# Optimization experiments

Measured on AMD Instinct MI355X. Metric: run time of the kernel, lower is better.

Reference implementation:

```python
import jax, jax.numpy as jnp
import numpy as np

N_NODES = 50000
N_EDGES = 800000
IN_DIM = 128
HEADS = 4
CH = 16            # hidden_dim per head
HC = HEADS * CH    # 64
N_GRAPHS = 64
NEG_SLOPE = 0.2


def gat_layer(x, edge_index, edge_attr, W, We, att_src, att_dst, att_edge, bias):
    """PyG GATConv (concat=True, edge_dim=1, eval mode: no dropout)."""
    N = x.shape[0]
    src, dst = edge_index[0], edge_index[1]
    xs = (x @ W).reshape(N, HEADS, CH)                         # [N,H,C]
    a_src = jnp.sum(xs * att_src, axis=-1)                     # [N,H]
    a_dst = jnp.sum(xs * att_dst, axis=-1)                     # [N,H]
    e = (edge_attr @ We).reshape(-1, HEADS, CH)                # [E,H,C]
    a_edge = jnp.sum(e * att_edge, axis=-1)                    # [E,H]
    alpha = a_src[src] + a_dst[dst] + a_edge                   # [E,H]
    alpha = jax.nn.leaky_relu(alpha, NEG_SLOPE)
    # segment softmax over incoming edges of each dst node
    seg_max = jax.ops.segment_max(alpha, dst, num_segments=N)  # [N,H]
    ealpha = jnp.exp(alpha - seg_max[dst])
    seg_sum = jax.ops.segment_sum(ealpha, dst, num_segments=N)
    coef = ealpha / seg_sum[dst]                               # [E,H]
    msg = xs[src] * coef[:, :, None]                           # [E,H,C]
    out = jax.ops.segment_sum(msg, dst, num_segments=N)        # [N,H,C]
    return out.reshape(N, HC) + bias


def setup_inputs() -> dict:
    key = jax.random.key(0)
    ks = jax.random.split(key, 20)
    s = 0.1
    inp = {
        "x": jax.random.normal(ks[0], (N_NODES, IN_DIM), dtype=jnp.float32),
        "edge_index": jax.random.randint(ks[1], (2, N_EDGES), 0, N_NODES, dtype=jnp.int32),
        "edge_attr": jax.random.normal(ks[2], (N_EDGES, 1), dtype=jnp.float32),
        "batch": jnp.sort(jax.random.randint(ks[3], (N_NODES,), 0, N_GRAPHS, dtype=jnp.int32)),
        # layer 1 params
        "W1": jax.random.normal(ks[4], (IN_DIM, HC), dtype=jnp.float32) * s,
        "We1": jax.random.normal(ks[5], (1, HC), dtype=jnp.float32) * s,
        "as1": jax.random.normal(ks[6], (HEADS, CH), dtype=jnp.float32) * s,
        "ad1": jax.random.normal(ks[7], (HEADS, CH), dtype=jnp.float32) * s,
        "ae1": jax.random.normal(ks[8], (HEADS, CH), dtype=jnp.float32) * s,
        "b1": jnp.zeros((HC,), dtype=jnp.float32),
        # layer 2 params (input HC)
        "W2": jax.random.normal(ks[9], (HC, HC), dtype=jnp.float32) * s,
        "We2": jax.random.normal(ks[10], (1, HC), dtype=jnp.float32) * s,
        "as2": jax.random.normal(ks[11], (HEADS, CH), dtype=jnp.float32) * s,
        "ad2": jax.random.normal(ks[12], (HEADS, CH), dtype=jnp.float32) * s,
        "ae2": jax.random.normal(ks[13], (HEADS, CH), dtype=jnp.float32) * s,
        "b2": jnp.zeros((HC,), dtype=jnp.float32),
    }
    return inp


def reference(x, edge_index, edge_attr, batch,
              W1, We1, as1, ad1, ae1, b1,
              W2, We2, as2, ad2, ae2, b2):
    h = gat_layer(x, edge_index, edge_attr, W1, We1, as1, ad1, ae1, b1)
    h = jax.nn.relu(h)                                          # dropout = identity (eval)
    h = gat_layer(h, edge_index, edge_attr, W2, We2, as2, ad2, ae2, b2)
    # global mean pool per graph
    sums = jax.ops.segment_sum(h, batch, num_segments=N_GRAPHS)           # [G,HC]
    cnt = jax.ops.segment_sum(jnp.ones((h.shape[0],), h.dtype), batch,
                              num_segments=N_GRAPHS)
    return sums / jnp.maximum(cnt, 1.0)[:, None]
```

## Files before the change

### kernel.cpp

```cpp
#include <hip/hip_runtime.h>
#include <hip/hip_fp16.h>
#include <float.h>

#define N_NODES   50000
#define N_EDGES   800000
#define INDIM1    128
#define HC        64
#define N_GRAPHS  64
#define NEG_SLOPE 0.2f
#define CAP       64
#define CSTRIDE   16

#define FGROUPS   521
#define FTBLK     (3 * FGROUPS)
#define FSBLK     (2 * FGROUPS)
#define FGRID     (5 * FGROUPS + 1)
#define ESTRIDE   (FSBLK * 256)

typedef _Float16 feat_t;

__global__ __launch_bounds__(256, 4) void fused1_kernel(const float* __restrict__ x,
                                                        const float* __restrict__ W,
                                                        const float* __restrict__ att_s,
                                                        const float* __restrict__ att_d,
                                                        feat_t* __restrict__ xs,
                                                        float* __restrict__ a_src,
                                                        float* __restrict__ a_dst,
                                                        const int* __restrict__ src,
                                                        const int* __restrict__ dst,
                                                        const float* __restrict__ eattr,
                                                        int* __restrict__ cursor,
                                                        unsigned int* __restrict__ csr_se,
                                                        const float* __restrict__ We1,
                                                        const float* __restrict__ ae1,
                                                        const float* __restrict__ We2,
                                                        const float* __restrict__ ae2,
                                                        float* __restrict__ wd) {
    constexpr int K4 = INDIM1 / 4;
    constexpr int NPW = 8;
    __shared__ float4 Wsh[K4 * 64];
    __shared__ float4 xsh[4][2][K4];
    int bid = blockIdx.x;
    int t = threadIdx.x;

    if (bid == FGRID - 1) {
        if (t < 128) {
            const float* We = (t < 64) ? We1 : We2;
            const float* ae = (t < 64) ? ae1 : ae2;
            int l = t & 63;
            float p = We[l] * ae[l];
            for (int off = 1; off < 16; off <<= 1) p += __shfl_xor(p, off);
            if ((l & 15) == 0) wd[(t >> 6) * 4 + (l >> 4)] = p;
        }
        return;
    }

    int grp = bid / 5;
    int rem = bid - grp * 5;
    if (rem >= 3) {
        int sb = grp * 2 + (rem - 3);
        for (int e = sb * 256 + t; e < N_EDGES; e += ESTRIDE) {
            int d = dst[e];
            int c = atomicAdd(&cursor[(size_t)d * CSTRIDE], 1);
            if (c < CAP) {
                unsigned int pk = (unsigned int)(src[e] & 0xFFFF)
                                | ((unsigned int)__half_as_ushort(__float2half(eattr[e])) << 16);
                csr_se[(size_t)d * CAP + c] = pk;
            }
        }
        return;
    }

    int tb = grp * 3 + rem;
    for (int i = t; i < K4 * 64; i += 256) {
        int k4 = i >> 6, col = i & 63;
        Wsh[i] = make_float4(W[(4 * k4 + 0) * 64 + col], W[(4 * k4 + 1) * 64 + col],
                             W[(4 * k4 + 2) * 64 + col], W[(4 * k4 + 3) * 64 + col]);
    }
    __syncthreads();
    int w = t >> 6, lane = t & 63;
    float avs = att_s[lane], avd = att_d[lane];
    int node0 = tb * (4 * NPW) + w * NPW;
    for (int ng = 0; ng < NPW; ng += 2) {
        int nbase = node0 + ng;
        if (nbase >= N_NODES) return;
        for (int q = lane; q < 2 * K4; q += 64) {
            int nn = q / K4, kk = q - nn * K4;
            int node = nbase + nn;
            xsh[w][nn][kk] = (node < N_NODES)
                ? ((const float4*)(x + (size_t)node * INDIM1))[kk]
                : make_float4(0.f, 0.f, 0.f, 0.f);
        }
        float acc0 = 0.f, acc1 = 0.f;
#pragma unroll 4
        for (int k4 = 0; k4 < K4; ++k4) {
            float4 wv = Wsh[k4 * 64 + lane];
            float4 x0 = xsh[w][0][k4];
            float4 x1 = xsh[w][1][k4];
            acc0 = fmaf(x0.x, wv.x, acc0);
            acc0 = fmaf(x0.y, wv.y, acc0);
            acc0 = fmaf(x0.z, wv.z, acc0);
            acc0 = fmaf(x0.w, wv.w, acc0);
            acc1 = fmaf(x1.x, wv.x, acc1);
            acc1 = fmaf(x1.y, wv.y, acc1);
            acc1 = fmaf(x1.z, wv.z, acc1);
            acc1 = fmaf(x1.w, wv.w, acc1);
        }
#pragma unroll
        for (int nn = 0; nn < 2; ++nn) {
            int node = nbase + nn;
            if (node >= N_NODES) break;
            float a = nn ? acc1 : acc0;
            xs[(size_t)node * 64 + lane] = (feat_t)a;
            float ps = a * avs;
            float pd = a * avd;
            for (int off = 1; off < 16; off <<= 1) {
                ps += __shfl_xor(ps, off);
                pd += __shfl_xor(pd, off);
            }
            if ((lane & 15) == 0) {
                a_src[node * 4 + (lane >> 4)] = ps;
                a_dst[node * 4 + (lane >> 4)] = pd;
            }
        }
    }
}

__global__ __launch_bounds__(256, 4) void agg1_kernel(const feat_t* __restrict__ xs,
                                                      const unsigned int* __restrict__ csr_se,
                                                      const int* __restrict__ degp,
                                                      const float* __restrict__ a_src,
                                                      const float* __restrict__ a_dst,
                                                      const float* __restrict__ wd,
                                                      const float* __restrict__ bias,
                                                      const float* __restrict__ W2,
                                                      const float* __restrict__ as2,
                                                      const float* __restrict__ ad2,
                                                      feat_t* __restrict__ xs2,
                                                      float* __restrict__ asrc2,
                                                      float* __restrict__ adst2) {
    __shared__ float W2sh[64 * 64];
    __shared__ float hshA[4][64];
    __shared__ float hshB[4][64];
    int t = threadIdx.x;
#pragma unroll
    for (int i = 0; i < 4; ++i)
        ((float4*)W2sh)[t + 256 * i] = ((const float4*)W2)[t + 256 * i];

    int w = t >> 6, lane = t & 63;
    const int e_idx = lane >> 2;
    const int h4 = lane & 3;
    const int h2 = lane >> 4;
    int nodeA = blockIdx.x * 8 + w * 2;
    int nodeB = nodeA + 1;

    float wdv = wd[h4];
    float bv = bias[lane];
    float avs2 = as2[lane], avd2 = ad2[lane];
    float advA = a_dst[nodeA * 4 + h4];
    float advB = a_dst[nodeB * 4 + h4];
    int nA = min(degp[(size_t)nodeA * CSTRIDE], CAP);
    int nB = min(degp[(size_t)nodeB * CSTRIDE], CAP);
    int begA = nodeA * CAP, endA = begA + nA;
    int begB = nodeB * CAP, endB = begB + nB;

    float mA = -FLT_MAX, sA = 0.f, accA = 0.f;
    float mB = -FLT_MAX, sB = 0.f, accB = 0.f;

    auto alpha_phase = [&](int beg, int end, int it, float adv,
                           float& m, float& s, float& acc, int& sv, float& wgt) {
        int j = beg + it * 16 + e_idx;
        bool v = j < end;
        sv = 0;
        float a = -FLT_MAX;
        if (v) {
            unsigned int se = csr_se[j];
            sv = (int)(se & 0xFFFFu);
            float ea = __half2float(__ushort_as_half((unsigned short)(se >> 16)));
            float as = a_src[sv * 4 + h4];
            a = as + adv + ea * wdv;
            a = a > 0.f ? a : NEG_SLOPE * a;
        }
        float cm = a;
        cm = fmaxf(cm, __shfl_xor(cm, 4));
        cm = fmaxf(cm, __shfl_xor(cm, 8));
        cm = fmaxf(cm, __shfl_xor(cm, 16));
        cm = fmaxf(cm, __shfl_xor(cm, 32));
        float mn = fmaxf(m, cm);
        float sc = __expf(m - mn);
        wgt = __expf(a - mn);
        s = s * sc + wgt;
        m = mn;
        acc *= __shfl(sc, h2);
    };
    auto gather_phase = [&](int sv, float wgt, float& acc) {
#pragma unroll
        for (int e = 0; e < 16; ++e) {
            int svb = __builtin_amdgcn_readlane(sv, e << 2);
            float wg = __shfl(wgt, (e << 2) | h2);
            acc = fmaf(wg, (float)xs[(size_t)svb * 64 + lane], acc);
        }
    };

    int itA = (nA + 15) >> 4, itB = (nB + 15) >> 4;
    int itC = min(itA, itB);
    for (int it = 0; it < itC; ++it) {
        int svA, svB; float wgtA, wgtB;
        alpha_phase(begA, endA, it, advA, mA, sA, accA, svA, wgtA);
        alpha_phase(begB, endB, it, advB, mB, sB, accB, svB, wgtB);
        gather_phase(svA, wgtA, accA);
        gather_phase(svB, wgtB, accB);
    }
    for (int it = itC; it < itA; ++it) {
        int svA; float wgtA;
        alpha_phase(begA, endA, it, advA, mA, sA, accA, svA, wgtA);
        gather_phase(svA, wgtA, accA);
    }
    for (int it = itC; it < itB; ++it) {
        int svB; float wgtB;
        alpha_phase(begB, endB, it, advB, mB, sB, accB, svB, wgtB);
        gather_phase(svB, wgtB, accB);
    }

    auto finish = [&](float s, float acc) {
        s += __shfl_xor(s, 4);
        s += __shfl_xor(s, 8);
        s += __shfl_xor(s, 16);
        s += __shfl_xor(s, 32);
        float sh = __shfl(s, h2);
        float res = (sh > 0.f) ? acc / sh : 0.f;
        return res + bv;
    };
    float hA = fmaxf(finish(sA, accA), 0.f);
    float hB = fmaxf(finish(sB, accB), 0.f);

    hshA[w][lane] = hA;
    hshB[w][lane] = hB;
    __syncthreads();

    float acc2A = 0.f, acc2B = 0.f;
#pragma unroll
    for (int k4 = 0; k4 < 16; ++k4) {
        float4 ha = ((const float4*)hshA[w])[k4];
        float4 hb = ((const float4*)hshB[w])[k4];
        float w0 = W2sh[(4 * k4 + 0) * 64 + lane];
        float w1 = W2sh[(4 * k4 + 1) * 64 + lane];
        float w2 = W2sh[(4 * k4 + 2) * 64 + lane];
        float w3 = W2sh[(4 * k4 + 3) * 64 + lane];
        acc2A = fmaf(ha.x, w0, acc2A); acc2B = fmaf(hb.x, w0, acc2B);
        acc2A = fmaf(ha.y, w1, acc2A); acc2B = fmaf(hb.y, w1, acc2B);
        acc2A = fmaf(ha.z, w2, acc2A); acc2B = fmaf(hb.z, w2, acc2B);
        acc2A = fmaf(ha.w, w3, acc2A); acc2B = fmaf(hb.w, w3, acc2B);
    }
    xs2[(size_t)nodeA * 64 + lane] = (feat_t)acc2A;
    xs2[(size_t)nodeB * 64 + lane] = (feat_t)acc2B;
    float psA = acc2A * avs2, pdA = acc2A * avd2;
    float psB = acc2B * avs2, pdB = acc2B * avd2;
    for (int off = 1; off < 16; off <<= 1) {
        psA += __shfl_xor(psA, off);
        pdA += __shfl_xor(pdA, off);
        psB += __shfl_xor(psB, off);
        pdB += __shfl_xor(pdB, off);
    }
    if ((lane & 15) == 0) {
        asrc2[nodeA * 4 + (lane >> 4)] = psA;
        adst2[nodeA * 4 + (lane >> 4)] = pdA;
        asrc2[nodeB * 4 + (lane >> 4)] = psB;
        adst2[nodeB * 4 + (lane >> 4)] = pdB;
    }
}

__global__ __launch_bounds__(256, 6) void agg2_kernel(const feat_t* __restrict__ xs,
                                                      const unsigned int* __restrict__ csr_se,
                                                      const int* __restrict__ degp,
                                                      const float* __restrict__ a_src,
                                                      const float* __restrict__ a_dst,
                                                      const float* __restrict__ wd,
                                                      const float* __restrict__ bias,
                                                      const int* __restrict__ batch,
                                                      float* __restrict__ gout) {
    __shared__ float plds[256];
    int t = threadIdx.x;
    int w = t >> 6, lane = t & 63;
    const int e_idx = lane >> 2;
    const int h4 = lane & 3;
    const int h2 = lane >> 4;
    int nodeA = blockIdx.x * 8 + w * 2;
    int nodeB = nodeA + 1;

    float wdv = wd[h4];
    float bv = bias[lane];
    float advA = a_dst[nodeA * 4 + h4];
    float advB = a_dst[nodeB * 4 + h4];
    int nA = min(degp[(size_t)nodeA * CSTRIDE], CAP);
    int nB = min(degp[(size_t)nodeB * CSTRIDE], CAP);
    int begA = nodeA * CAP, endA = begA + nA;
    int begB = nodeB * CAP, endB = begB + nB;

    float mA = -FLT_MAX, sA = 0.f, accA = 0.f;
    float mB = -FLT_MAX, sB = 0.f, accB = 0.f;

    auto alpha_phase = [&](int beg, int end, int it, float adv,
                           float& m, float& s, float& acc, int& sv, float& wgt) {
        int j = beg + it * 16 + e_idx;
        bool v = j < end;
        sv = 0;
        float a = -FLT_MAX;
        if (v) {
            unsigned int se = csr_se[j];
            sv = (int)(se & 0xFFFFu);
            float ea = __half2float(__ushort_as_half((unsigned short)(se >> 16)));
            float as = a_src[sv * 4 + h4];
            a = as + adv + ea * wdv;
            a = a > 0.f ? a : NEG_SLOPE * a;
        }
        float cm = a;
        cm = fmaxf(cm, __shfl_xor(cm, 4));
        cm = fmaxf(cm, __shfl_xor(cm, 8));
        cm = fmaxf(cm, __shfl_xor(cm, 16));
        cm = fmaxf(cm, __shfl_xor(cm, 32));
        float mn = fmaxf(m, cm);
        float sc = __expf(m - mn);
        wgt = __expf(a - mn);
        s = s * sc + wgt;
        m = mn;
        acc *= __shfl(sc, h2);
    };
    auto gather_phase = [&](int sv, float wgt, float& acc) {
#pragma unroll
        for (int e = 0; e < 16; ++e) {
            int svb = __builtin_amdgcn_readlane(sv, e << 2);
            float wg = __shfl(wgt, (e << 2) | h2);
            acc = fmaf(wg, (float)xs[(size_t)svb * 64 + lane], acc);
        }
    };

    int itA = (nA + 15) >> 4, itB = (nB + 15) >> 4;
    int itC = min(itA, itB);
    for (int it = 0; it < itC; ++it) {
        int svA, svB; float wgtA, wgtB;
        alpha_phase(begA, endA, it, advA, mA, sA, accA, svA, wgtA);
        alpha_phase(begB, endB, it, advB, mB, sB, accB, svB, wgtB);
        gather_phase(svA, wgtA, accA);
        gather_phase(svB, wgtB, accB);
    }
    for (int it = itC; it < itA; ++it) {
        int svA; float wgtA;
        alpha_phase(begA, endA, it, advA, mA, sA, accA, svA, wgtA);
        gather_phase(svA, wgtA, accA);
    }
    for (int it = itC; it < itB; ++it) {
        int svB; float wgtB;
        alpha_phase(begB, endB, it, advB, mB, sB, accB, svB, wgtB);
        gather_phase(svB, wgtB, accB);
    }

    auto finish = [&](float s, float acc) {
        s += __shfl_xor(s, 4);
        s += __shfl_xor(s, 8);
        s += __shfl_xor(s, 16);
        s += __shfl_xor(s, 32);
        float sh = __shfl(s, h2);
        float res = (sh > 0.f) ? acc / sh : 0.f;
        return res + bv;
    };
    float resA = finish(sA, accA);
    float resB = finish(sB, accB);

    int gA = batch[nodeA], gB = batch[nodeB];
    int gF = batch[blockIdx.x * 8];
    int gL = batch[blockIdx.x * 8 + 7];
    if (gF == gL) {
        plds[w * 64 + lane] = resA + resB;
        __syncthreads();
        if (w == 0) {
            float v = plds[lane] + plds[64 + lane] +
                      plds[128 + lane] + plds[192 + lane];
            atomicAdd(&gout[gF * 64 + lane], v);
        }
    } else {
        if (gA == gB) {
            atomicAdd(&gout[gA * 64 + lane], resA + resB);
        } else {
            atomicAdd(&gout[gA * 64 + lane], resA);
            atomicAdd(&gout[gB * 64 + lane], resB);
        }
    }
}

__global__ void pool_div_kernel(float* __restrict__ out, const int* __restrict__ batch) {
    int g = blockIdx.x, t = threadIdx.x;
    int lo = 0, hi = N_NODES;
    while (lo < hi) { int mid = (lo + hi) >> 1; if (batch[mid] < g) lo = mid + 1; else hi = mid; }
    int lo2 = lo, hi2 = N_NODES;
    while (lo2 < hi2) { int mid = (lo2 + hi2) >> 1; if (batch[mid] <= g) lo2 = mid + 1; else hi2 = mid; }
    float c = (float)max(lo2 - lo, 1);
    out[g * 64 + t] /= c;
}


extern "C" void kernel_launch(void* const* d_in, const int* in_sizes, int n_in,
                              void* d_out, int out_size, void* d_ws, size_t ws_size,
                              hipStream_t stream) {
    const float* x    = (const float*)d_in[0];
    const int*   eidx = (const int*)d_in[1];
    const float* eat  = (const float*)d_in[2];
    const int*   batch= (const int*)d_in[3];
    const float* W1   = (const float*)d_in[4];
    const float* We1  = (const float*)d_in[5];
    const float* as1  = (const float*)d_in[6];
    const float* ad1  = (const float*)d_in[7];
    const float* ae1  = (const float*)d_in[8];
    const float* b1   = (const float*)d_in[9];
    const float* W2   = (const float*)d_in[10];
    const float* We2  = (const float*)d_in[11];
    const float* as2  = (const float*)d_in[12];
    const float* ad2  = (const float*)d_in[13];
    const float* ae2  = (const float*)d_in[14];
    const float* b2   = (const float*)d_in[15];
    const int* src  = eidx;
    const int* dstp = eidx + N_EDGES;
    float* out = (float*)d_out;

    char* p = (char*)d_ws;
    auto alloc = [&](size_t bytes) {
        char* r = p;
        p += (bytes + 255) & ~(size_t)255;
        return r;
    };
    unsigned int* csrse = (unsigned int*)alloc((size_t)N_NODES * CAP * 4);
    feat_t* xs     = (feat_t*)alloc((size_t)N_NODES * 64 * 2);
    feat_t* hbuf   = (feat_t*)alloc((size_t)N_NODES * 64 * 2);
    float*  asrc   = (float*)alloc((size_t)N_NODES * 4 * 4);
    float*  adst   = (float*)alloc((size_t)N_NODES * 4 * 4);
    float*  asrc2  = (float*)alloc((size_t)N_NODES * 4 * 4);
    float*  adst2  = (float*)alloc((size_t)N_NODES * 4 * 4);
    float*  wd     = (float*)alloc(64);
    int*    cursor = (int*)alloc((size_t)N_NODES * CSTRIDE * 4);

    hipMemsetAsync(cursor, 0, (size_t)N_NODES * CSTRIDE * 4, stream);
    hipMemsetAsync(d_out, 0, (size_t)N_GRAPHS * 64 * 4, stream);

    const int NB = N_NODES / 8;

    fused1_kernel<<<FGRID, 256, 0, stream>>>(x, W1, as1, ad1, xs, asrc, adst,
                                             src, dstp, eat, cursor, csrse,
                                             We1, ae1, We2, ae2, wd);
    agg1_kernel<<<NB, 256, 0, stream>>>(xs, csrse, cursor, asrc, adst,
                                        wd, b1, W2, as2, ad2,
                                        hbuf, asrc2, adst2);
    agg2_kernel<<<NB, 256, 0, stream>>>(hbuf, csrse, cursor, asrc2, adst2,
                                        wd + 4, b2, batch, out);
    pool_div_kernel<<<N_GRAPHS, 64, 0, stream>>>(out, batch);
}
```

Before: 233.7 us.

## Replace online softmax loop with fully unrolled two-pass aggregation over capped edges

The aggregation loops of both GAT layers used an iterative online softmax with per-chunk rescaling, and each chunk's gather waited on that chunk's alpha. They are now fully unrolled over the four possible 16-edge chunks (CAP=64). All alpha values and the max are computed first, then the exponentials and sum, then the gathers into four independent accumulators. This exposes more independent loads and removes the rescale dependency chain, at the cost of many more live registers. agg2's launch bounds drop from 6 to 4 waves to allow for that.

```diff
diff --git a/kernel.cpp b/kernel.cpp
--- a/kernel.cpp
+++ b/kernel.cpp
@@ -126,6 +126,80 @@
     }
 }
 
+#define ALPHA_IT(N, I)                                                          \
+    {                                                                           \
+        int j = beg##N + I * 16 + e_idx;                                        \
+        float a = -FLT_MAX;                                                     \
+        if (j < end##N) {                                                       \
+            unsigned int se = csr_se[j];                                        \
+            sv##N##I = (int)(se & 0xFFFFu);                                     \
+            float ea = __half2float(__ushort_as_half((unsigned short)(se >> 16)));\
+            float as = a_src[sv##N##I * 4 + h4];                                \
+            a = as + adv##N + ea * wdv;                                         \
+            a = a > 0.f ? a : NEG_SLOPE * a;                                    \
+        }                                                                       \
+        w##N##I = a;                                                            \
+        float cm = a;                                                           \
+        cm = fmaxf(cm, __shfl_xor(cm, 4));                                      \
+        cm = fmaxf(cm, __shfl_xor(cm, 8));                                      \
+        cm = fmaxf(cm, __shfl_xor(cm, 16));                                     \
+        cm = fmaxf(cm, __shfl_xor(cm, 32));                                     \
+        m##N = fmaxf(m##N, cm);                                                 \
+    }
+
+#define GATHER_IT(N, I)                                                         \
+    {                                                                           \
+        _Pragma("unroll")                                                       \
+        for (int e = 0; e < 16; ++e) {                                          \
+            int svb = __builtin_amdgcn_readlane(sv##N##I, e << 2);              \
+            float wg = __shfl(w##N##I, (e << 2) | h2);                          \
+            acc##N##I = fmaf(wg, (float)xs[(size_t)svb * 64 + lane], acc##N##I);\
+        }                                                                       \
+    }
+
+#define AGG_CORE                                                                \
+    int svA0 = 0, svA1 = 0, svA2 = 0, svA3 = 0;                                 \
+    int svB0 = 0, svB1 = 0, svB2 = 0, svB3 = 0;                                 \
+    float wA0 = -FLT_MAX, wA1 = -FLT_MAX, wA2 = -FLT_MAX, wA3 = -FLT_MAX;       \
+    float wB0 = -FLT_MAX, wB1 = -FLT_MAX, wB2 = -FLT_MAX, wB3 = -FLT_MAX;       \
+    float mA = -FLT_MAX, mB = -FLT_MAX;                                         \
+    if (nA > 0)  ALPHA_IT(A, 0)                                                 \
+    if (nB > 0)  ALPHA_IT(B, 0)                                                 \
+    if (nA > 16) ALPHA_IT(A, 1)                                                 \
+    if (nB > 16) ALPHA_IT(B, 1)                                                 \
+    if (nA > 32) ALPHA_IT(A, 2)                                                 \
+    if (nB > 32) ALPHA_IT(B, 2)                                                 \
+    if (nA > 48) ALPHA_IT(A, 3)                                                 \
+    if (nB > 48) ALPHA_IT(B, 3)                                                 \
+    float mmA = (nA > 0) ? mA : 0.f;                \
+    float mmB = (nB > 0) ? mB : 0.f;                                            \
+    wA0 = __expf(wA0 - mmA); wA1 = __expf(wA1 - mmA);                           \
+    wA2 = __expf(wA2 - mmA); wA3 = __expf(wA3 - mmA);                           \
+    wB0 = __expf(wB0 - mmB); wB1 = __expf(wB1 - mmB);                           \
+    wB2 = __expf(wB2 - mmB); wB3 = __expf(wB3 - mmB);                           \
+    float sA = (wA0 + wA1) + (wA2 + wA3);                                       \
+    float sB = (wB0 + wB1) + (wB2 + wB3);                                       \
+    sA += __shfl_xor(sA, 4);  sB += __shfl_xor(sB, 4);                          \
+    sA += __shfl_xor(sA, 8);  sB += __shfl_xor(sB, 8);                          \
+    sA += __shfl_xor(sA, 16); sB += __shfl_xor(sB, 16);                         \
+    sA += __shfl_xor(sA, 32); sB += __shfl_xor(sB, 32);                         \
+    float accA0 = 0.f, accA1 = 0.f, accA2 = 0.f, accA3 = 0.f;                   \
+    float accB0 = 0.f, accB1 = 0.f, accB2 = 0.f, accB3 = 0.f;                   \
+    if (nA > 0)  GATHER_IT(A, 0)                                                \
+    if (nB > 0)  GATHER_IT(B, 0)                                                \
+    if (nA > 16) GATHER_IT(A, 1)                                                \
+    if (nB > 16) GATHER_IT(B, 1)                                                \
+    if (nA > 32) GATHER_IT(A, 2)                                                \
+    if (nB > 32) GATHER_IT(B, 2)                                                \
+    if (nA > 48) GATHER_IT(A, 3)                                                \
+    if (nB > 48) GATHER_IT(B, 3)                                                \
+    float accA = (accA0 + accA1) + (accA2 + accA3);                             \
+    float accB = (accB0 + accB1) + (accB2 + accB3);                             \
+    float shA = __shfl(sA, h2);                                                 \
+    float shB = __shfl(sB, h2);                                                 \
+    float resA = ((shA > 0.f) ? accA / shA : 0.f) + bv;                         \
+    float resB = ((shB > 0.f) ? accB / shB : 0.f) + bv;
+
 __global__ __launch_bounds__(256, 4) void agg1_kernel(const feat_t* __restrict__ xs,
                                                       const unsigned int* __restrict__ csr_se,
                                                       const int* __restrict__ degp,
@@ -164,75 +238,10 @@
     int begA = nodeA * CAP, endA = begA + nA;
     int begB = nodeB * CAP, endB = begB + nB;
 
-    float mA = -FLT_MAX, sA = 0.f, accA = 0.f;
-    float mB = -FLT_MAX, sB = 0.f, accB = 0.f;
-
-    auto alpha_phase = [&](int beg, int end, int it, float adv,
-                           float& m, float& s, float& acc, int& sv, float& wgt) {
-        int j = beg + it * 16 + e_idx;
-        bool v = j < end;
-        sv = 0;
-        float a = -FLT_MAX;
-        if (v) {
-            unsigned int se = csr_se[j];
-            sv = (int)(se & 0xFFFFu);
-            float ea = __half2float(__ushort_as_half((unsigned short)(se >> 16)));
-            float as = a_src[sv * 4 + h4];
-            a = as + adv + ea * wdv;
-            a = a > 0.f ? a : NEG_SLOPE * a;
-        }
-        float cm = a;
-        cm = fmaxf(cm, __shfl_xor(cm, 4));
-        cm = fmaxf(cm, __shfl_xor(cm, 8));
-        cm = fmaxf(cm, __shfl_xor(cm, 16));
-        cm = fmaxf(cm, __shfl_xor(cm, 32));
-        float mn = fmaxf(m, cm);
-        float sc = __expf(m - mn);
-        wgt = __expf(a - mn);
-        s = s * sc + wgt;
-        m = mn;
-        acc *= __shfl(sc, h2);
-    };
-    auto gather_phase = [&](int sv, float wgt, float& acc) {
-#pragma unroll
-        for (int e = 0; e < 16; ++e) {
-            int svb = __builtin_amdgcn_readlane(sv, e << 2);
-            float wg = __shfl(wgt, (e << 2) | h2);
-            acc = fmaf(wg, (float)xs[(size_t)svb * 64 + lane], acc);
-        }
-    };
-
-    int itA = (nA + 15) >> 4, itB = (nB + 15) >> 4;
-    int itC = min(itA, itB);
-    for (int it = 0; it < itC; ++it) {
-        int svA, svB; float wgtA, wgtB;
-        alpha_phase(begA, endA, it, advA, mA, sA, accA, svA, wgtA);
-        alpha_phase(begB, endB, it, advB, mB, sB, accB, svB, wgtB);
-        gather_phase(svA, wgtA, accA);
-        gather_phase(svB, wgtB, accB);
-    }
-    for (int it = itC; it < itA; ++it) {
-        int svA; float wgtA;
-        alpha_phase(begA, endA, it, advA, mA, sA, accA, svA, wgtA);
-        gather_phase(svA, wgtA, accA);
-    }
-    for (int it = itC; it < itB; ++it) {
-        int svB; float wgtB;
-        alpha_phase(begB, endB, it, advB, mB, sB, accB, svB, wgtB);
-        gather_phase(svB, wgtB, accB);
-    }
-
-    auto finish = [&](float s, float acc) {
-        s += __shfl_xor(s, 4);
-        s += __shfl_xor(s, 8);
-        s += __shfl_xor(s, 16);
-        s += __shfl_xor(s, 32);
-        float sh = __shfl(s, h2);
-        float res = (sh > 0.f) ? acc / sh : 0.f;
-        return res + bv;
-    };
-    float hA = fmaxf(finish(sA, accA), 0.f);
-    float hB = fmaxf(finish(sB, accB), 0.f);
+    AGG_CORE
+
+    float hA = fmaxf(resA, 0.f);
+    float hB = fmaxf(resB, 0.f);
 
     hshA[w][lane] = hA;
     hshB[w][lane] = hB;
@@ -270,7 +279,7 @@
     }
 }
 
-__global__ __launch_bounds__(256, 6) void agg2_kernel(const feat_t* __restrict__ xs,
+__global__ __launch_bounds__(256, 4) void agg2_kernel(const feat_t* __restrict__ xs,
                                                       const unsigned int* __restrict__ csr_se,
                                                       const int* __restrict__ degp,
                                                       const float* __restrict__ a_src,
@@ -297,75 +306,7 @@
     int begA = nodeA * CAP, endA = begA + nA;
     int begB = nodeB * CAP, endB = begB + nB;
 
-    float mA = -FLT_MAX, sA = 0.f, accA = 0.f;
-    float mB = -FLT_MAX, sB = 0.f, accB = 0.f;
-
-    auto alpha_phase = [&](int beg, int end, int it, float adv,
-                           float& m, float& s, float& acc, int& sv, float& wgt) {
-        int j = beg + it * 16 + e_idx;
-        bool v = j < end;
-        sv = 0;
-        float a = -FLT_MAX;
-        if (v) {
-            unsigned int se = csr_se[j];
-            sv = (int)(se & 0xFFFFu);
-            float ea = __half2float(__ushort_as_half((unsigned short)(se >> 16)));
-            float as = a_src[sv * 4 + h4];
-            a = as + adv + ea * wdv;
-            a = a > 0.f ? a : NEG_SLOPE * a;
-        }
-        float cm = a;
-        cm = fmaxf(cm, __shfl_xor(cm, 4));
-        cm = fmaxf(cm, __shfl_xor(cm, 8));
-        cm = fmaxf(cm, __shfl_xor(cm, 16));
-        cm = fmaxf(cm, __shfl_xor(cm, 32));
-        float mn = fmaxf(m, cm);
-        float sc = __expf(m - mn);
-        wgt = __expf(a - mn);
-        s = s * sc + wgt;
-        m = mn;
-        acc *= __shfl(sc, h2);
-    };
-    auto gather_phase = [&](int sv, float wgt, float& acc) {
-#pragma unroll
-        for (int e = 0; e < 16; ++e) {
-            int svb = __builtin_amdgcn_readlane(sv, e << 2);
-            float wg = __shfl(wgt, (e << 2) | h2);
-            acc = fmaf(wg, (float)xs[(size_t)svb * 64 + lane], acc);
-        }
-    };
-
-    int itA = (nA + 15) >> 4, itB = (nB + 15) >> 4;
-    int itC = min(itA, itB);
-    for (int it = 0; it < itC; ++it) {
-        int svA, svB; float wgtA, wgtB;
-        alpha_phase(begA, endA, it, advA, mA, sA, accA, svA, wgtA);
-        alpha_phase(begB, endB, it, advB, mB, sB, accB, svB, wgtB);
-        gather_phase(svA, wgtA, accA);
-        gather_phase(svB, wgtB, accB);
-    }
-    for (int it = itC; it < itA; ++it) {
-        int svA; float wgtA;
-        alpha_phase(begA, endA, it, advA, mA, sA, accA, svA, wgtA);
-        gather_phase(svA, wgtA, accA);
-    }
-    for (int it = itC; it < itB; ++it) {
-        int svB; float wgtB;
-        alpha_phase(begB, endB, it, advB, mB, sB, accB, svB, wgtB);
-        gather_phase(svB, wgtB, accB);
-    }
-
-    auto finish = [&](float s, float acc) {
-        s += __shfl_xor(s, 4);
-        s += __shfl_xor(s, 8);
-        s += __shfl_xor(s, 16);
-        s += __shfl_xor(s, 32);
-        float sh = __shfl(s, h2);
-        float res = (sh > 0.f) ? acc / sh : 0.f;
-        return res + bv;
-    };
-    float resA = finish(sA, accA);
-    float resB = finish(sB, accB);
+    AGG_CORE
 
     int gA = batch[nodeA], gB = batch[nodeB];
     int gF = batch[blockIdx.x * 8];
```

Result: faster. 224.9 us (median of 2 runs) (-3.7%).
